# Kernel tuning notes

Hardware: AMD Instinct MI355X
Metric: run time of the kernel (lower is better)

## Reference

```python
import jax, jax.numpy as jnp
import numpy as np

NODE = 112
B = 4096
L1, L2, L3, L4 = 256, 256, 128, 64


def setup_inputs() -> dict:
    key = jax.random.key(0)
    ks = jax.random.split(key, 13)
    def lin(kw, kb, fan_in, fan_out):
        bound = 1.0 / np.sqrt(fan_in)
        W = jax.random.uniform(kw, (fan_out, fan_in), jnp.float32, -bound, bound)
        b = jax.random.uniform(kb, (fan_out,), jnp.float32, -bound, bound)
        return W, b
    x = jax.random.normal(ks[0], (B, NODE, NODE), jnp.float32)
    W1, b1 = lin(ks[1], ks[2], NODE, L1)
    W2, b2 = lin(ks[3], ks[4], L1, L2)
    W3, b3 = lin(ks[5], ks[6], L2, L3)
    W4, b4 = lin(ks[7], ks[8], L3, L4)
    W5, b5 = lin(ks[9], ks[10], L4, 1)
    Wf, bf = lin(ks[11], ks[12], NODE, 1)
    return {"x": x, "W1": W1, "b1": b1, "W2": W2, "b2": b2,
            "W3": W3, "b3": b3, "W4": W4, "b4": b4,
            "W5": W5, "b5": b5, "Wf": Wf, "bf": bf}


def reference(x, W1, b1, W2, b2, W3, b3, W4, b4, W5, b5, Wf, bf):
    # bmm(x, eye) == x, so first aggregation is the identity on x.
    h = x  # [B, node, node]
    # layer: aggregate via x, project, relu
    def layer(h, W, b):
        h = jnp.einsum('bnm,bmd->bnd', x, h)  # adjacency aggregation
        return jax.nn.relu(h @ W.T + b)
    h = jax.nn.relu(h @ W1.T + b1)            # first bmm is identity
    h = layer(h, W2, b2)
    h = layer(h, W3, b3)
    h = layer(h, W4, b4)
    h = layer(h, W5, b5)                      # [B, node, 1]
    h = h.reshape(h.shape[0], -1)             # [B, node]
    return h @ Wf.T + bf                      # [B, 1]
```

## Files before the change

### kernel.cpp

```cpp
#include <hip/hip_runtime.h>
#include <hip/hip_bf16.h>


#define NODE 112
#define NBATCH 4096
#define SXS 120
#define AB_OFF (96*SXS)
#define SMEM_BYTES ((AB_OFF + 112*256)*2)

typedef float  f4v   __attribute__((ext_vector_type(4)));
typedef float  f16v  __attribute__((ext_vector_type(16)));
typedef __bf16 bf8v  __attribute__((ext_vector_type(8)));
typedef short  s8v   __attribute__((ext_vector_type(8)));
typedef unsigned u4v __attribute__((ext_vector_type(4)));
typedef unsigned short ushort_t;

__device__ __forceinline__ ushort_t f2bf(float f) {
  union { float f; unsigned u; } v; v.f = f;
  unsigned r = v.u + 0x7FFFu + ((v.u >> 16) & 1u);
  return (ushort_t)(r >> 16);
}
__device__ __forceinline__ float bf2f(ushort_t h) {
  union { unsigned u; float f; } v; v.u = ((unsigned)h) << 16; return v.f;
}
__device__ __forceinline__ unsigned pk2(float a, float b) {
  unsigned short ul = __builtin_bit_cast(unsigned short, (__bf16)a);
  unsigned short uh = __builtin_bit_cast(unsigned short, (__bf16)b);
  return (unsigned)ul | ((unsigned)uh << 16);
}
__device__ __forceinline__ bf8v ld_frag(const ushort_t* p) {
  s8v t = *(const s8v*)p;
  return __builtin_bit_cast(bf8v, t);
}
__device__ __forceinline__ unsigned xchg32(unsigned v, int lane) {
  return (unsigned)__builtin_amdgcn_ds_bpermute(((lane ^ 32) << 2), (int)v);
}
#define MFMA32(a,b,c) __builtin_amdgcn_mfma_f32_32x32x16_bf16((a),(b),(c),0,0,0)

template<int M>
__device__ __forceinline__ void exch_m(const f16v& acc, float bv, int lane,
                                       unsigned* fr)
{
  const bool hiH = (lane >> 5) != 0;
  unsigned P[4][2];
  const int NQ = (M==3) ? 2 : 4;
  #pragma unroll
  for (int q=0;q<4;q++) {
    if (q >= NQ) break;
    float v0 = fmaxf(acc[4*q+0]+bv, 0.f);
    float v1 = fmaxf(acc[4*q+1]+bv, 0.f);
    float v2 = fmaxf(acc[4*q+2]+bv, 0.f);
    float v3 = fmaxf(acc[4*q+3]+bv, 0.f);
    P[q][0] = pk2(v0, v1);
    P[q][1] = pk2(v2, v3);
  }
  {
    unsigned s0 = hiH ? P[0][0] : P[1][0];
    unsigned s1 = hiH ? P[0][1] : P[1][1];
    unsigned r0 = xchg32(s0, lane);
    unsigned r1 = xchg32(s1, lane);
    unsigned o0 = hiH ? P[1][0] : P[0][0];
    unsigned o1 = hiH ? P[1][1] : P[0][1];
    fr[8*M+0] = hiH ? r0 : o0;
    fr[8*M+1] = hiH ? r1 : o1;
    fr[8*M+2] = hiH ? o0 : r0;
    fr[8*M+3] = hiH ? o1 : r1;
  }
  if (M < 3) {
    unsigned s0 = hiH ? P[2][0] : P[3][0];
    unsigned s1 = hiH ? P[2][1] : P[3][1];
    unsigned r0 = xchg32(s0, lane);
    unsigned r1 = xchg32(s1, lane);
    unsigned o0 = hiH ? P[3][0] : P[2][0];
    unsigned o1 = hiH ? P[3][1] : P[2][1];
    fr[8*M+4] = hiH ? r0 : o0;
    fr[8*M+5] = hiH ? r1 : o1;
    fr[8*M+6] = hiH ? o0 : r0;
    fr[8*M+7] = hiH ? o1 : r1;
  }
}

__device__ __forceinline__ void exch_build(const f16v* acc, float bv, int lane,
                                           unsigned* fr)
{
  exch_m<0>(acc[0], bv, lane, fr);
  exch_m<1>(acc[1], bv, lane, fr);
  exch_m<2>(acc[2], bv, lane, fr);
  exch_m<3>(acc[3], bv, lane, fr);
}

__device__ __forceinline__ void proj1_exch(
    const ushort_t* Xs, const bf8v* Xr3, const ushort_t* __restrict__ Wg,
    const float* __restrict__ bias, int nt, int lane, unsigned* fr)
{
  const int l31 = lane & 31, h32 = lane >> 5;
  f16v acc[4];
  #pragma unroll
  for (int m=0;m<4;m++)
    #pragma unroll
    for (int r=0;r<16;r++) acc[m][r] = 0.f;

  const ushort_t* aP = Xs + l31*SXS + h32*8;
  const ushort_t* bP = Wg + (nt*32 + l31)*112 + h32*8;
  #pragma unroll
  for (int ks=0; ks<7; ks++) {
    bf8v B = ld_frag(bP + ks*16);
    acc[0] = MFMA32(ld_frag(aP +          ks*16), B, acc[0]);
    acc[1] = MFMA32(ld_frag(aP + 32*SXS + ks*16), B, acc[1]);
    acc[2] = MFMA32(ld_frag(aP + 64*SXS + ks*16), B, acc[2]);
    acc[3] = MFMA32(Xr3[ks], B, acc[3]);
  }
  exch_build(acc, bias[nt*32 + l31], lane, fr);
}

template<int KS>
__device__ __forceinline__ void proj_exch(
    const ushort_t* aBs, const ushort_t* __restrict__ Wg, int WK,
    const float* __restrict__ bias, int nt, int lane, int sw, unsigned* fr)
{
  const int l31 = lane & 31, h32 = lane >> 5;
  f16v acc[4];
  #pragma unroll
  for (int m=0;m<4;m++)
    #pragma unroll
    for (int r=0;r<16;r++) acc[m][r] = 0.f;

  const int r0 = l31*256, r1 = (32+l31)*256, r2 = (64+l31)*256;
  const int r3 = (96 + (l31 & 15))*256;
  const ushort_t* bP = Wg + (nt*32 + l31)*WK + h32*8;
  #pragma unroll
  for (int ks=0; ks<KS; ks++) {
    bf8v B = ld_frag(bP + ks*16);
    const int c = (16*ks + 8*h32) ^ sw;
    acc[0] = MFMA32(ld_frag(aBs + r0 + c), B, acc[0]);
    acc[1] = MFMA32(ld_frag(aBs + r1 + c), B, acc[1]);
    acc[2] = MFMA32(ld_frag(aBs + r2 + c), B, acc[2]);
    acc[3] = MFMA32(ld_frag(aBs + r3 + c), B, acc[3]);
  }
  exch_build(acc, bias[nt*32 + l31], lane, fr);
}

template<int KS, int M0>
__device__ __forceinline__ void proj_pass(
    const ushort_t* aBs, const ushort_t* __restrict__ Wg, int WK,
    const float* __restrict__ bias, int nt, int lane, int sw, unsigned* fr)
{
  const int l31 = lane & 31, h32 = lane >> 5;
  f16v acc0, acc1;
  #pragma unroll
  for (int r=0;r<16;r++) { acc0[r] = 0.f; acc1[r] = 0.f; }

  const int r0 = ((M0==0 ? 0 : 64) + l31)*256;
  const int r1 = (M0==0) ? (32 + l31)*256 : (96 + (l31 & 15))*256;
  const ushort_t* bP = Wg + (nt*32 + l31)*WK + h32*8;
  #pragma unroll
  for (int ks=0; ks<KS; ks++) {
    bf8v B = ld_frag(bP + ks*16);
    const int c = (16*ks + 8*h32) ^ sw;
    acc0 = MFMA32(ld_frag(aBs + r0 + c), B, acc0);
    acc1 = MFMA32(ld_frag(aBs + r1 + c), B, acc1);
  }
  const float bv = bias[nt*32 + l31];
  exch_m<M0>(acc0, bv, lane, fr);
  exch_m<M0+1>(acc1, bv, lane, fr);
}

template<int N0>
__device__ __forceinline__ void agg_half(
    const unsigned* fr, const ushort_t* Xs, const bf8v* Xr3,
    ushort_t* aBs, int mt, int lane, int sw)
{
  const int l31 = lane & 31, h32 = lane >> 5;
  f16v acc0, acc1;
  #pragma unroll
  for (int r=0;r<16;r++) { acc0[r] = 0.f; acc1[r] = 0.f; }

  const ushort_t* bP = Xs + l31*SXS + h32*8;
  #pragma unroll
  for (int ks=0; ks<7; ks++) {
    u4v t = (u4v){fr[4*ks+0], fr[4*ks+1], fr[4*ks+2], fr[4*ks+3]};
    bf8v A = __builtin_bit_cast(bf8v, t);
    bf8v B0 = ld_frag(bP + N0*32*SXS + ks*16);
    bf8v B1 = (N0 == 0) ? ld_frag(bP + 32*SXS + ks*16) : Xr3[ks];
    acc0 = MFMA32(A, B0, acc0);
    acc1 = MFMA32(A, B1, acc1);
  }

  #pragma unroll
  for (int s=0;s<2;s++) {
    const f16v& a = s ? acc1 : acc0;
    const int n = N0 + s;
    const int row = (n < 3) ? (n*32 + l31) : (96 + l31);
    const bool on = (n < 3) || (l31 < 16);
    #pragma unroll
    for (int q=0;q<4;q++) {
      uint2 pv;
      pv.x = pk2(a[4*q+0], a[4*q+1]);
      pv.y = pk2(a[4*q+2], a[4*q+3]);
      const int col = (mt*32 + 8*q + 4*h32) ^ sw;
      if (on) *(uint2*)(aBs + row*256 + col) = pv;
    }
  }
}

__global__ void prep_weights(const float* __restrict__ W1, const float* __restrict__ W2,
                             const float* __restrict__ W3, const float* __restrict__ W4,
                             ushort_t* __restrict__ o)
{
  int i = blockIdx.x*256 + threadIdx.x;
  if (i < 28672)       o[i] = f2bf(W1[i]);
  else if (i < 94208)  o[i] = f2bf(W2[i - 28672]);
  else if (i < 126976) o[i] = f2bf(W3[i - 94208]);
  else if (i < 135168) o[i] = f2bf(W4[i - 126976]);
}

__global__ void __launch_bounds__(256, 2) gcn_kernel(
    const float* __restrict__ x, const ushort_t* __restrict__ wsp,
    const float* __restrict__ b1, const float* __restrict__ b2,
    const float* __restrict__ b3, const float* __restrict__ b4,
    const float* __restrict__ W5, const float* __restrict__ b5,
    const float* __restrict__ Wf, const float* __restrict__ bfc,
    float* __restrict__ out)
{
  extern __shared__ ushort_t smem[];
  ushort_t* Xs = smem;
  ushort_t* aB = smem + AB_OFF;

  const int tid  = threadIdx.x;
  const int w    = tid >> 6;
  const int lane = tid & 63;
  const int l31  = lane & 31, h32 = lane >> 5;
  const int sw   = (l31 & 7) << 3;

  {
    const float4* x4 = (const float4*)(x + (size_t)blockIdx.x * (NODE*NODE));
    for (int i = tid; i < (NODE*NODE/4); i += 256) {
      float4 v = x4[i];
      int r = i / 28, c4 = (i - r*28) * 4;
      uint2 pv; pv.x = pk2(v.x, v.y); pv.y = pk2(v.z, v.w);
      ushort_t* dst = (r < 96) ? (Xs + r*SXS + c4) : (aB + (r-96)*SXS + c4);
      *(uint2*)dst = pv;
    }
  }
  __syncthreads();

  bf8v Xr3[7];
  {
    const ushort_t* sp = aB + (l31 & 15)*SXS + h32*8;
    #pragma unroll
    for (int ks=0;ks<7;ks++) Xr3[ks] = ld_frag(sp + ks*16);
  }
  __syncthreads();

  unsigned frA[28], frB[28];

  proj1_exch(Xs, Xr3, wsp, b1, w, lane, frA);
  agg_half<0>(frA, Xs, Xr3, aB, w, lane, sw);
  agg_half<2>(frA, Xs, Xr3, aB, w, lane, sw);
  proj1_exch(Xs, Xr3, wsp, b1, w+4, lane, frB);
  agg_half<0>(frB, Xs, Xr3, aB, w+4, lane, sw);
  agg_half<2>(frB, Xs, Xr3, aB, w+4, lane, sw);
  __syncthreads();

  proj_pass<16,0>(aB, wsp + 28672, 256, b2, w,   lane, sw, frA);
  proj_pass<16,2>(aB, wsp + 28672, 256, b2, w,   lane, sw, frA);
  proj_pass<16,0>(aB, wsp + 28672, 256, b2, w+4, lane, sw, frB);
  proj_pass<16,2>(aB, wsp + 28672, 256, b2, w+4, lane, sw, frB);
  __syncthreads();
  agg_half<0>(frA, Xs, Xr3, aB, w,   lane, sw);
  agg_half<2>(frA, Xs, Xr3, aB, w,   lane, sw);
  agg_half<0>(frB, Xs, Xr3, aB, w+4, lane, sw);
  agg_half<2>(frB, Xs, Xr3, aB, w+4, lane, sw);
  __syncthreads();

  proj_exch<16>(aB, wsp + 94208, 256, b3, w, lane, sw, frA);
  __syncthreads();
  agg_half<0>(frA, Xs, Xr3, aB, w, lane, sw);
  agg_half<2>(frA, Xs, Xr3, aB, w, lane, sw);
  __syncthreads();

  if (w < 2) proj_exch<8>(aB, wsp + 126976, 128, b4, w, lane, sw, frA);
  __syncthreads();
  if (w < 2) {
    agg_half<0>(frA, Xs, Xr3, aB, w, lane, sw);
    agg_half<2>(frA, Xs, Xr3, aB, w, lane, sw);
  }
  __syncthreads();

  float partial = 0.f;
  if (tid < NODE) {
    const int swr = (tid & 7) << 3;
    const ushort_t* row = aB + tid*256;
    float s = 0.f;
    #pragma unroll
    for (int k4 = 0; k4 < 16; k4++) {
      uint2 u = *(const uint2*)(row + ((4*k4) ^ swr));
      s += bf2f((ushort_t)(u.x & 0xFFFF)) * W5[k4*4+0];
      s += bf2f((ushort_t)(u.x >> 16))    * W5[k4*4+1];
      s += bf2f((ushort_t)(u.y & 0xFFFF)) * W5[k4*4+2];
      s += bf2f((ushort_t)(u.y >> 16))    * W5[k4*4+3];
    }
    s += b5[0];
    s = s > 0.f ? s : 0.f;
    partial = s * Wf[tid];
  }
  float* red = (float*)Xs;
  if (tid < 128) red[tid] = partial;
  __syncthreads();
  if (w == 0) {
    float v = red[lane] + red[lane + 64];
    #pragma unroll
    for (int off = 32; off > 0; off >>= 1)
      v += __shfl_xor(v, off, 64);
    if (lane == 0) out[blockIdx.x] = v + bfc[0];
  }
}

extern "C" void kernel_launch(void* const* d_in, const int* in_sizes, int n_in,
                              void* d_out, int out_size, void* d_ws, size_t ws_size,
                              hipStream_t stream) {
  const float* x   = (const float*)d_in[0];
  const float* W1  = (const float*)d_in[1];
  const float* b1  = (const float*)d_in[2];
  const float* W2  = (const float*)d_in[3];
  const float* b2  = (const float*)d_in[4];
  const float* W3  = (const float*)d_in[5];
  const float* b3  = (const float*)d_in[6];
  const float* W4  = (const float*)d_in[7];
  const float* b4  = (const float*)d_in[8];
  const float* W5  = (const float*)d_in[9];
  const float* b5  = (const float*)d_in[10];
  const float* Wf  = (const float*)d_in[11];
  const float* bfc = (const float*)d_in[12];
  ushort_t* wsp = (ushort_t*)d_ws;
  float* out = (float*)d_out;

  prep_weights<<<528, 256, 0, stream>>>(W1, W2, W3, W4, wsp);

  (void)hipFuncSetAttribute((const void*)gcn_kernel,
                            hipFuncAttributeMaxDynamicSharedMemorySize, SMEM_BYTES);
  gcn_kernel<<<NBATCH, 256, SMEM_BYTES, stream>>>(x, wsp, b1, b2, b3, b4,
                                                  W5, b5, Wf, bfc, out);
}
```

Before: 535.7 us.

## Permute node columns of x and W1 to remove cross-half lane exchanges

```diff
diff --git a/kernel.cpp b/kernel.cpp
--- a/kernel.cpp
+++ b/kernel.cpp
@@ -32,61 +32,27 @@
   s8v t = *(const s8v*)p;
   return __builtin_bit_cast(bf8v, t);
 }
-__device__ __forceinline__ unsigned xchg32(unsigned v, int lane) {
-  return (unsigned)__builtin_amdgcn_ds_bpermute(((lane ^ 32) << 2), (int)v);
+__device__ __forceinline__ int nu4(int c) {
+  return (c & ~12) | ((c & 4) << 1) | ((c & 8) >> 1);
 }
 #define MFMA32(a,b,c) __builtin_amdgcn_mfma_f32_32x32x16_bf16((a),(b),(c),0,0,0)
 
 template<int M>
-__device__ __forceinline__ void exch_m(const f16v& acc, float bv, int lane,
-                                       unsigned* fr)
-{
-  const bool hiH = (lane >> 5) != 0;
-  unsigned P[4][2];
-  const int NQ = (M==3) ? 2 : 4;
-  #pragma unroll
-  for (int q=0;q<4;q++) {
-    if (q >= NQ) break;
-    float v0 = fmaxf(acc[4*q+0]+bv, 0.f);
-    float v1 = fmaxf(acc[4*q+1]+bv, 0.f);
-    float v2 = fmaxf(acc[4*q+2]+bv, 0.f);
-    float v3 = fmaxf(acc[4*q+3]+bv, 0.f);
-    P[q][0] = pk2(v0, v1);
-    P[q][1] = pk2(v2, v3);
-  }
-  {
-    unsigned s0 = hiH ? P[0][0] : P[1][0];
-    unsigned s1 = hiH ? P[0][1] : P[1][1];
-    unsigned r0 = xchg32(s0, lane);
-    unsigned r1 = xchg32(s1, lane);
-    unsigned o0 = hiH ? P[1][0] : P[0][0];
-    unsigned o1 = hiH ? P[1][1] : P[0][1];
-    fr[8*M+0] = hiH ? r0 : o0;
-    fr[8*M+1] = hiH ? r1 : o1;
-    fr[8*M+2] = hiH ? o0 : r0;
-    fr[8*M+3] = hiH ? o1 : r1;
-  }
-  if (M < 3) {
-    unsigned s0 = hiH ? P[2][0] : P[3][0];
-    unsigned s1 = hiH ? P[2][1] : P[3][1];
-    unsigned r0 = xchg32(s0, lane);
-    unsigned r1 = xchg32(s1, lane);
-    unsigned o0 = hiH ? P[3][0] : P[2][0];
-    unsigned o1 = hiH ? P[3][1] : P[2][1];
-    fr[8*M+4] = hiH ? r0 : o0;
-    fr[8*M+5] = hiH ? r1 : o1;
-    fr[8*M+6] = hiH ? o0 : r0;
-    fr[8*M+7] = hiH ? o1 : r1;
-  }
-}
-
-__device__ __forceinline__ void exch_build(const f16v* acc, float bv, int lane,
-                                           unsigned* fr)
-{
-  exch_m<0>(acc[0], bv, lane, fr);
-  exch_m<1>(acc[1], bv, lane, fr);
-  exch_m<2>(acc[2], bv, lane, fr);
-  exch_m<3>(acc[3], bv, lane, fr);
+__device__ __forceinline__ void pack_m(const f16v& acc, float bv, unsigned* fr)
+{
+  #pragma unroll
+  for (int k = 0; k < ((M==3) ? 4 : 8); k++) {
+    float v0 = fmaxf(acc[2*k+0]+bv, 0.f);
+    float v1 = fmaxf(acc[2*k+1]+bv, 0.f);
+    fr[8*M+k] = pk2(v0, v1);
+  }
+}
+__device__ __forceinline__ void pack_build(const f16v* acc, float bv, unsigned* fr)
+{
+  pack_m<0>(acc[0], bv, fr);
+  pack_m<1>(acc[1], bv, fr);
+  pack_m<2>(acc[2], bv, fr);
+  pack_m<3>(acc[3], bv, fr);
 }
 
 __device__ __forceinline__ void proj1_exch(
@@ -110,7 +76,7 @@
     acc[2] = MFMA32(ld_frag(aP + 64*SXS + ks*16), B, acc[2]);
     acc[3] = MFMA32(Xr3[ks], B, acc[3]);
   }
-  exch_build(acc, bias[nt*32 + l31], lane, fr);
+  pack_build(acc, bias[nt*32 + l31], fr);
 }
 
 template<int KS>
@@ -137,7 +103,7 @@
     acc[2] = MFMA32(ld_frag(aBs + r2 + c), B, acc[2]);
     acc[3] = MFMA32(ld_frag(aBs + r3 + c), B, acc[3]);
   }
-  exch_build(acc, bias[nt*32 + l31], lane, fr);
+  pack_build(acc, bias[nt*32 + l31], fr);
 }
 
 template<int KS, int M0>
@@ -161,8 +127,8 @@
     acc1 = MFMA32(ld_frag(aBs + r1 + c), B, acc1);
   }
   const float bv = bias[nt*32 + l31];
-  exch_m<M0>(acc0, bv, lane, fr);
-  exch_m<M0+1>(acc1, bv, lane, fr);
+  pack_m<M0>(acc0, bv, fr);
+  pack_m<M0+1>(acc1, bv, fr);
 }
 
 template<int N0>
@@ -208,7 +174,10 @@
                              ushort_t* __restrict__ o)
 {
   int i = blockIdx.x*256 + threadIdx.x;
-  if (i < 28672)       o[i] = f2bf(W1[i]);
+  if (i < 28672) {
+    int src = (i & ~12) | ((i & 4) << 1) | ((i & 8) >> 1);
+    o[i] = f2bf(W1[src]);
+  }
   else if (i < 94208)  o[i] = f2bf(W2[i - 28672]);
   else if (i < 126976) o[i] = f2bf(W3[i - 94208]);
   else if (i < 135168) o[i] = f2bf(W4[i - 126976]);
@@ -237,6 +206,7 @@
     for (int i = tid; i < (NODE*NODE/4); i += 256) {
       float4 v = x4[i];
       int r = i / 28, c4 = (i - r*28) * 4;
+      c4 = nu4(c4);
       uint2 pv; pv.x = pk2(v.x, v.y); pv.y = pk2(v.z, v.w);
       ushort_t* dst = (r < 96) ? (Xs + r*SXS + c4) : (aB + (r-96)*SXS + c4);
       *(uint2*)dst = pv;
```

After: 535.6 us. Within noise of the previous version (-0.0%).
